# Performance work log

Measured on AMD Instinct MI355X. Metric: run time of the kernel, lower is better.

## Reference

```python
import jax, jax.numpy as jnp
import numpy as np

N, E, DIM, H = 50000, 800000, 128, 8
HD = DIM // H  # head_dim = 16
HID = 4 * DIM  # ffn hidden (hidden_dim_multiplier=4)


def setup_inputs() -> dict:
    key = jax.random.key(0)
    ks = jax.random.split(key, 12)
    s = 0.05
    return {
        "x": jax.random.normal(ks[0], (N, DIM), jnp.float32),
        "src": jax.random.randint(ks[1], (E,), 0, N, jnp.int32),
        "dst": jax.random.randint(ks[2], (E,), 0, N, jnp.int32),
        "fc_w": jax.random.normal(ks[3], (DIM, DIM), jnp.float32) * s,
        "fc_b": jax.random.normal(ks[4], (DIM,), jnp.float32) * s,
        "au_w": jax.random.normal(ks[5], (H, DIM), jnp.float32) * s,
        "au_b": jax.random.normal(ks[6], (H,), jnp.float32) * s,
        "av_w": jax.random.normal(ks[7], (H, DIM), jnp.float32) * s,
        "w1": jax.random.normal(ks[8], (HID, 4 * DIM), jnp.float32) * s,
        "b1": jax.random.normal(ks[9], (HID,), jnp.float32) * s,
        "w2": jax.random.normal(ks[10], (DIM, HID), jnp.float32) * s,
        "b2": jax.random.normal(ks[11], (DIM,), jnp.float32) * s,
    }


def reference(x, src, dst, fc_w, fc_b, au_w, au_b, av_w, w1, b1, w2, b2):
    h = x @ fc_w.T + fc_b                                   # [N, DIM]
    su = h @ au_w.T + au_b                                  # [N, H]
    sv = h @ av_w.T                                         # [N, H] (no bias)
    # u_add_v + LeakyReLU(0.2)
    scores = jax.nn.leaky_relu(su[src] + sv[dst], 0.2)      # [E, H]
    # edge_softmax grouped by destination node (stable)
    m = jax.ops.segment_max(scores, dst, num_segments=N)    # [N, H]
    ex = jnp.exp(scores - m[dst])
    den = jax.ops.segment_sum(ex, dst, num_segments=N)      # [N, H]
    probs = ex / den[dst]                                   # [E, H]
    # u_mul_e_sum over heads: x reshaped [N, head_dim, H]
    xh = h.reshape(N, HD, H)
    msg = jax.ops.segment_sum(xh[src] * probs[:, None, :], dst, num_segments=N)
    msg = msg.reshape(N, DIM)
    # copy_u_mean: mean of src features over incoming edges
    ones = jnp.ones((E,), h.dtype)
    in_deg = jax.ops.segment_sum(ones, dst, num_segments=N)   # [N]
    sum2 = jax.ops.segment_sum(xh[src], dst, num_segments=N)  # [N, HD, H]
    msg2 = (sum2 / jnp.maximum(in_deg, 1.0)[:, None, None]).reshape(N, DIM)
    # symmetric-norm message: norm = 1/sqrt(out_deg[src]*out_deg[dst])
    out_deg = jax.ops.segment_sum(ones, src, num_segments=N)  # [N]
    norm = 1.0 / jnp.sqrt(out_deg[src] * out_deg[dst])        # [E]
    msg3 = jax.ops.segment_sum(h[src] * norm[:, None], dst, num_segments=N)
    # combine + feed-forward (dropout=0 -> identity)
    cat = jnp.concatenate([h, msg, msg2, msg3], axis=1)       # [N, 4*DIM]
    f = jax.nn.gelu(cat @ w1.T + b1, approximate=False)
    return f @ w2.T + b2                                      # [N, DIM]
```

## Files before the change

kernel.cpp:

```cpp
#include <hip/hip_runtime.h>
#include <hip/hip_bf16.h>

#define NNODES 50000
#define NEDGES 800000
#define DIM 128
#define NH 8
#define HID 512
#define NB 196

typedef unsigned short ushort_t;
typedef unsigned int uint_t;
typedef __attribute__((ext_vector_type(8))) short bf16x8;
typedef __attribute__((ext_vector_type(4))) float f32x4;

__global__ __launch_bounds__(256) void convert_weights_kernel(
    const float* __restrict__ fc_w, const float* __restrict__ w1,
    const float* __restrict__ w2,
    ushort_t* __restrict__ fc_wb, ushort_t* __restrict__ w1b,
    ushort_t* __restrict__ w2b)
{
    int i = blockIdx.x * 256 + threadIdx.x;
    if (i < 16384)
        ((__hip_bfloat16*)fc_wb)[i] = __float2bfloat16(fc_w[i]);
    else if (i < 278528)
        ((__hip_bfloat16*)w1b)[i - 16384] = __float2bfloat16(w1[i - 16384]);
    else if (i < 344064)
        ((__hip_bfloat16*)w2b)[i - 278528] = __float2bfloat16(w2[i - 278528]);
}

template<int AF32, int OUTF32, int ACT>
__global__ __launch_bounds__(256, 4) void gemm_mfma(
    const void* A, int lda,
    const ushort_t* __restrict__ B, int ldb,
    const float* __restrict__ bias,
    void* C, int ldc, int row0,
    int M, int K)
{
    constexpr int BM = 128, BN = 128, BK = 32;
    __shared__ ushort_t As[BM * BK];
    __shared__ ushort_t Bs[BN * BK];

    const int t    = threadIdx.x;
    const int bm   = blockIdx.y * BM;
    const int bn   = blockIdx.x * BN;
    const int wid  = t >> 6, lane = t & 63;
    const int wrow = wid >> 1, wcol = wid & 1;
    const int qd   = lane >> 4, l16 = lane & 15;

    f32x4 acc[4][4];
#pragma unroll
    for (int i = 0; i < 4; ++i)
#pragma unroll
        for (int j = 0; j < 4; ++j) acc[i][j] = (f32x4){0.f, 0.f, 0.f, 0.f};

    for (int k0 = 0; k0 < K; k0 += BK) {
#pragma unroll
        for (int it = 0; it < 2; ++it) {
            const int v = it * 256 + t;
            const int r = v >> 2, q = v & 3;
            const int c = q ^ ((r >> 1) & 3);
            {
                const ushort_t* gB = B + (size_t)(bn + r) * ldb + k0 + c * 8;
                ushort_t* lB = &Bs[(it * 256 + wid * 64) * 8];
                __builtin_amdgcn_global_load_lds(
                    (const __attribute__((address_space(1))) uint_t*)gB,
                    (__attribute__((address_space(3))) uint_t*)lB, 16, 0, 0);
            }
            if (AF32) {
                int gr = bm + r;
                float4 f0 = make_float4(0.f, 0.f, 0.f, 0.f), f1 = f0;
                if (gr < M) {
                    const float* ap = (const float*)A + (size_t)gr * lda + k0 + c * 8;
                    f0 = *(const float4*)ap;
                    f1 = *(const float4*)(ap + 4);
                }
                __hip_bfloat16 tmp[8];
                tmp[0] = __float2bfloat16(f0.x); tmp[1] = __float2bfloat16(f0.y);
                tmp[2] = __float2bfloat16(f0.z); tmp[3] = __float2bfloat16(f0.w);
                tmp[4] = __float2bfloat16(f1.x); tmp[5] = __float2bfloat16(f1.y);
                tmp[6] = __float2bfloat16(f1.z); tmp[7] = __float2bfloat16(f1.w);
                *(uint4*)&As[(r * 4 + q) * 8] = *(const uint4*)tmp;
            } else {
                int gr = bm + r;
                if (gr >= M) gr = M - 1;
                const ushort_t* gA = (const ushort_t*)A + (size_t)gr * lda + k0 + c * 8;
                ushort_t* lA = &As[(it * 256 + wid * 64) * 8];
                __builtin_amdgcn_global_load_lds(
                    (const __attribute__((address_space(1))) uint_t*)gA,
                    (__attribute__((address_space(3))) uint_t*)lA, 16, 0, 0);
            }
        }
        __syncthreads();

        bf16x8 af[4], bfr[4];
#pragma unroll
        for (int mi = 0; mi < 4; ++mi) {
            const int row = wrow * 64 + mi * 16 + l16;
            af[mi] = *(const bf16x8*)&As[row * BK + ((qd ^ ((row >> 1) & 3)) * 8)];
        }
#pragma unroll
        for (int ni = 0; ni < 4; ++ni) {
            const int row = wcol * 64 + ni * 16 + l16;
            bfr[ni] = *(const bf16x8*)&Bs[row * BK + ((qd ^ ((row >> 1) & 3)) * 8)];
        }
#pragma unroll
        for (int mi = 0; mi < 4; ++mi)
#pragma unroll
            for (int ni = 0; ni < 4; ++ni)
                acc[mi][ni] = __builtin_amdgcn_mfma_f32_16x16x32_bf16(
                    af[mi], bfr[ni], acc[mi][ni], 0, 0, 0);
        __syncthreads();
    }

#pragma unroll
    for (int mi = 0; mi < 4; ++mi) {
#pragma unroll
        for (int r = 0; r < 4; ++r) {
            int lrow = wrow * 64 + mi * 16 + qd * 4 + r;
            int grow = bm + lrow;
            if (grow >= M) continue;
#pragma unroll
            for (int ni = 0; ni < 4; ++ni) {
                int gc = bn + wcol * 64 + ni * 16 + l16;
                float v = acc[mi][ni][r] + bias[gc];
                if (ACT == 1) v = 0.5f * v * (1.f + erff(v * 0.70710678118654752f));
                size_t off = (size_t)(row0 + grow) * ldc + gc;
                if (OUTF32) ((float*)C)[off] = v;
                else ((__hip_bfloat16*)C)[off] = __float2bfloat16(v);
            }
        }
    }
}

__global__ __launch_bounds__(256) void attn_scores_kernel(
    const ushort_t* __restrict__ hb,
    const float* __restrict__ au_w, const float* __restrict__ au_b,
    const float* __restrict__ av_w,
    float* __restrict__ su, float* __restrict__ sv, int N)
{
    const int wave = threadIdx.x >> 6;
    const int lane = threadIdx.x & 63;
    const int n = blockIdx.x * 4 + wave;
    if (n >= N) return;

    const float h0 = __bfloat162float(((const __hip_bfloat16*)hb)[(size_t)n * DIM + lane]);
    const float h1 = __bfloat162float(((const __hip_bfloat16*)hb)[(size_t)n * DIM + 64 + lane]);

    float au[NH], av[NH];
#pragma unroll
    for (int hh = 0; hh < NH; ++hh) {
        au[hh] = h0 * au_w[hh * DIM + lane] + h1 * au_w[hh * DIM + 64 + lane];
        av[hh] = h0 * av_w[hh * DIM + lane] + h1 * av_w[hh * DIM + 64 + lane];
    }
#pragma unroll
    for (int off = 32; off >= 1; off >>= 1) {
#pragma unroll
        for (int hh = 0; hh < NH; ++hh) {
            au[hh] += __shfl_down(au[hh], off, 64);
            av[hh] += __shfl_down(av[hh], off, 64);
        }
    }
    if (lane == 0) {
#pragma unroll
        for (int hh = 0; hh < NH; ++hh) {
            su[(size_t)n * NH + hh] = au[hh] + au_b[hh];
            sv[(size_t)n * NH + hh] = av[hh];
        }
    }
}

__global__ __launch_bounds__(256) void degree_count_kernel(
    const int* __restrict__ src, const int* __restrict__ dst,
    float* __restrict__ out_deg, int* __restrict__ in_cnt, int E)
{
    int e = blockIdx.x * 256 + threadIdx.x;
    if (e >= E) return;
    unsafeAtomicAdd(&out_deg[src[e]], 1.f);
    atomicAdd(&in_cnt[dst[e]], 1);
}

__global__ __launch_bounds__(256) void block_sum_kernel(
    const int* __restrict__ cnt, int* __restrict__ bsum)
{
    const int lane = threadIdx.x & 63, wid = threadIdx.x >> 6;
    int i = blockIdx.x * 256 + threadIdx.x;
    int v = (i < NNODES) ? cnt[i] : 0;
#pragma unroll
    for (int off = 32; off >= 1; off >>= 1) v += __shfl_down(v, off, 64);
    __shared__ int ws_[4];
    if (lane == 0) ws_[wid] = v;
    __syncthreads();
    if (threadIdx.x == 0) bsum[blockIdx.x] = ws_[0] + ws_[1] + ws_[2] + ws_[3];
}

__global__ __launch_bounds__(256) void block_scan_kernel(
    const int* __restrict__ bsum, int* __restrict__ boff)
{
    __shared__ int sb[256];
    const int t = threadIdx.x;
    int v = (t < NB) ? bsum[t] : 0;
    sb[t] = v;
    __syncthreads();
    for (int off = 1; off < 256; off <<= 1) {
        int u = (t >= off) ? sb[t - off] : 0;
        __syncthreads();
        sb[t] += u;
        __syncthreads();
    }
    if (t < NB) boff[t] = (t == 0) ? 0 : sb[t - 1];
}

__global__ __launch_bounds__(256) void final_scan_kernel(
    const int* __restrict__ cnt, const int* __restrict__ boff,
    int* __restrict__ rowstart)
{
    __shared__ int sb[256];
    const int t = threadIdx.x;
    const int b = blockIdx.x;
    int i = b * 256 + t;
    int v = (i < NNODES) ? cnt[i] : 0;
    sb[t] = v;
    __syncthreads();
    for (int off = 1; off < 256; off <<= 1) {
        int u = (t >= off) ? sb[t - off] : 0;
        __syncthreads();
        sb[t] += u;
        __syncthreads();
    }
    if (i < NNODES) rowstart[i] = boff[b] + sb[t] - v;
    if (b == 0 && t == 0) rowstart[NNODES] = NEDGES;
}

__global__ __launch_bounds__(256) void fill_csr_kernel(
    const int* __restrict__ src, const int* __restrict__ dst,
    const int* __restrict__ rowstart, int* __restrict__ cursor,
    int* __restrict__ esrc, int E)
{
    int e = blockIdx.x * 256 + threadIdx.x;
    if (e >= E) return;
    int d = dst[e];
    int pos = rowstart[d] + atomicAdd(&cursor[d], 1);
    esrc[pos] = src[e];
}

__device__ __forceinline__ float bf_lo(uint_t v) {
    union { uint_t i; float f; } c; c.i = v << 16; return c.f;
}
__device__ __forceinline__ float bf_hi(uint_t v) {
    union { uint_t i; float f; } c; c.i = v & 0xffff0000u; return c.f;
}
__device__ __forceinline__ void st_bf2(ushort_t* p, float a, float b) {
    __hip_bfloat16 ba = __float2bfloat16(a), bb = __float2bfloat16(b);
    uint_t v = (uint_t)(*(ushort_t*)&ba) | ((uint_t)(*(ushort_t*)&bb) << 16);
    *(uint_t*)p = v;
}

__global__ __launch_bounds__(256) void gather_aggregate_kernel(
    const int* __restrict__ rowstart, const int* __restrict__ esrc,
    const ushort_t* __restrict__ hb,
    const float* __restrict__ su, const float* __restrict__ sv,
    const float* __restrict__ out_deg,
    ushort_t* __restrict__ cat, int N)
{
    const int wave = threadIdx.x >> 6;
    const int lane = threadIdx.x & 63;
    const int n = blockIdx.x * 4 + wave;
    if (n >= N) return;

    const int d0 = lane << 1;
    const int h0 = d0 & 7;

    const int e0  = rowstart[n];
    const int deg = rowstart[n + 1] - e0;
    const float2 svv = *(const float2*)(sv + (size_t)n * NH + h0);
    const float od_d = out_deg[n];

    int es = 0;
    if (deg > 0) es = esrc[e0 + (lane < deg ? lane : deg - 1)];

    float den0 = 0.f, den1 = 0.f;
    float m0 = 0.f, m1 = 0.f, s0 = 0.f, s1 = 0.f, n0 = 0.f, n1 = 0.f;

    const int degm = deg & ~3;
    for (int j = 0; j < degm; j += 4) {
        int s4[4]; float2 su4[4]; float od4[4]; uint_t hv4[4];
#pragma unroll
        for (int u = 0; u < 4; ++u) {
            int jj = j + u;
            s4[u] = (jj < 64) ? __shfl(es, jj, 64) : esrc[e0 + jj];
        }
#pragma unroll
        for (int u = 0; u < 4; ++u) {
            su4[u] = *(const float2*)(su + (size_t)s4[u] * NH + h0);
            od4[u] = out_deg[s4[u]];
            hv4[u] = *(const uint_t*)(hb + (size_t)s4[u] * DIM + d0);
        }
#pragma unroll
        for (int u = 0; u < 4; ++u) {
            float sc0 = su4[u].x + svv.x; sc0 = sc0 < 0.f ? 0.2f * sc0 : sc0;
            float sc1 = su4[u].y + svv.y; sc1 = sc1 < 0.f ? 0.2f * sc1 : sc1;
            float ex0 = __expf(sc0), ex1 = __expf(sc1);
            den0 += ex0; den1 += ex1;
            float nrm = rsqrtf(od4[u] * od_d);
            float hs0 = bf_lo(hv4[u]), hs1 = bf_hi(hv4[u]);
            m0 += hs0 * ex0; m1 += hs1 * ex1;
            s0 += hs0;       s1 += hs1;
            n0 += hs0 * nrm; n1 += hs1 * nrm;
        }
    }
    for (int j = degm; j < deg; ++j) {
        int s = (j < 64) ? __shfl(es, j, 64) : esrc[e0 + j];
        float2 suv = *(const float2*)(su + (size_t)s * NH + h0);
        float odv  = out_deg[s];
        uint_t hv  = *(const uint_t*)(hb + (size_t)s * DIM + d0);
        float sc0 = suv.x + svv.x; sc0 = sc0 < 0.f ? 0.2f * sc0 : sc0;
        float sc1 = suv.y + svv.y; sc1 = sc1 < 0.f ? 0.2f * sc1 : sc1;
        float ex0 = __expf(sc0), ex1 = __expf(sc1);
        den0 += ex0; den1 += ex1;
        float nrm = rsqrtf(odv * od_d);
        float hs0 = bf_lo(hv), hs1 = bf_hi(hv);
        m0 += hs0 * ex0; m1 += hs1 * ex1;
        s0 += hs0;       s1 += hs1;
        n0 += hs0 * nrm; n1 += hs1 * nrm;
    }

    const float inv = 1.f / fmaxf((float)deg, 1.f);
    const float r0 = den0 > 0.f ? 1.f / den0 : 0.f;
    const float r1 = den1 > 0.f ? 1.f / den1 : 0.f;
    ushort_t* row = cat + (size_t)n * 512;
    *(uint_t*)(row + d0) = *(const uint_t*)(hb + (size_t)n * DIM + d0);
    st_bf2(row + 128 + d0, m0 * r0, m1 * r1);
    st_bf2(row + 256 + d0, s0 * inv, s1 * inv);
    st_bf2(row + 384 + d0, n0, n1);
}

extern "C" void kernel_launch(void* const* d_in, const int* in_sizes, int n_in,
                              void* d_out, int out_size, void* d_ws, size_t ws_size,
                              hipStream_t stream)
{
    const float* x    = (const float*)d_in[0];
    const int*   src  = (const int*)d_in[1];
    const int*   dst  = (const int*)d_in[2];
    const float* fc_w = (const float*)d_in[3];
    const float* fc_b = (const float*)d_in[4];
    const float* au_w = (const float*)d_in[5];
    const float* au_b = (const float*)d_in[6];
    const float* av_w = (const float*)d_in[7];
    const float* w1   = (const float*)d_in[8];
    const float* b1   = (const float*)d_in[9];
    const float* w2   = (const float*)d_in[10];
    const float* b2   = (const float*)d_in[11];
    float* out = (float*)d_out;

    const int N = NNODES, E = NEDGES;

    char* w = (char*)d_ws;
    ushort_t* fc_wb = (ushort_t*)w;  w += (size_t)DIM * DIM * 2;
    ushort_t* w1b   = (ushort_t*)w;  w += (size_t)HID * 512 * 2;
    ushort_t* w2b   = (ushort_t*)w;  w += (size_t)DIM * HID * 2;
    ushort_t* hb    = (ushort_t*)w;  w += (size_t)N * DIM * 2;
    ushort_t* cat   = (ushort_t*)w;  w += (size_t)N * 512 * 2;
    float* su       = (float*)w;     w += (size_t)N * NH * 4;
    float* sv       = (float*)w;     w += (size_t)N * NH * 4;
    float* out_deg  = (float*)w;     w += (size_t)N * 4;
    int*   in_cnt   = (int*)w;       w += (size_t)N * 4;
    int*   cursor   = (int*)w;       w += (size_t)N * 4;
    int*   rowstart = (int*)w;       w += (size_t)(N + 16) * 4;
    int*   bsum     = (int*)w;       w += (size_t)256 * 4;
    int*   boff     = (int*)w;       w += (size_t)256 * 4;
    int*   esrc     = (int*)w;       w += (size_t)E * 4;
    size_t base_bytes = (size_t)(w - (char*)d_ws);
    ushort_t* fbuf  = (ushort_t*)w;

    const int CHR = (ws_size >= base_bytes + (size_t)N * 512 * 2 + 1024) ? N : 12500;

    (void)hipMemsetAsync(out_deg, 0, (size_t)N * 3 * 4, stream);

    convert_weights_kernel<<<1344, 256, 0, stream>>>(fc_w, w1, w2, fc_wb, w1b, w2b);

    {
        dim3 g(1, (N + 127) / 128);
        gemm_mfma<1, 0, 0><<<g, 256, 0, stream>>>(x, DIM, fc_wb, DIM, fc_b,
                                                  hb, DIM, 0, N, DIM);
    }
    attn_scores_kernel<<<(N + 3) / 4, 256, 0, stream>>>(hb, au_w, au_b, av_w, su, sv, N);
    degree_count_kernel<<<(E + 255) / 256, 256, 0, stream>>>(src, dst, out_deg, in_cnt, E);
    block_sum_kernel<<<NB, 256, 0, stream>>>(in_cnt, bsum);
    block_scan_kernel<<<1, 256, 0, stream>>>(bsum, boff);
    final_scan_kernel<<<NB, 256, 0, stream>>>(in_cnt, boff, rowstart);
    fill_csr_kernel<<<(E + 255) / 256, 256, 0, stream>>>(src, dst, rowstart, cursor, esrc, E);
    gather_aggregate_kernel<<<(N + 3) / 4, 256, 0, stream>>>(
        rowstart, esrc, hb, su, sv, out_deg, cat, N);

    for (int c0 = 0; c0 < N; c0 += CHR) {
        int Mc = (c0 + CHR <= N) ? CHR : N - c0;
        {
            dim3 g(HID / 128, (Mc + 127) / 128);
            gemm_mfma<0, 0, 1><<<g, 256, 0, stream>>>(cat + (size_t)c0 * 512, 512,
                                                      w1b, 512, b1,
                                                      fbuf, HID, 0, Mc, 512);
        }
        {
            dim3 g(DIM / 128, (Mc + 127) / 128);
            gemm_mfma<0, 1, 0><<<g, 256, 0, stream>>>(fbuf, HID, w2b, HID, b2,
                                                      out, DIM, c0, Mc, 512);
        }
    }
}
```

Baseline: 425.5 us.

## Triple-buffer bf16 GEMM LDS loads with async prefetch and drop XOR swizzle

The bf16-input GEMM path now keeps three LDS buffers and prefetches tiles two k-steps ahead with global_load_lds. It waits with explicit vmcnt counts and uses one barrier per iteration instead of two, so global loads overlap MFMA work. The XOR swizzle on LDS layout is removed from both paths, which simplifies addressing but may add LDS bank conflicts. Occupancy hint drops from 4 to 3 blocks because shared memory grows threefold.

```diff
diff --git a/kernel.cpp b/kernel.cpp
--- a/kernel.cpp
+++ b/kernel.cpp
@@ -12,6 +12,9 @@
 typedef unsigned int uint_t;
 typedef __attribute__((ext_vector_type(8))) short bf16x8;
 typedef __attribute__((ext_vector_type(4))) float f32x4;
+
+#define WAITVM4 asm volatile("s_waitcnt vmcnt(4)" ::: "memory")
+#define WAITVM0 asm volatile("s_waitcnt vmcnt(0)" ::: "memory")
 
 __global__ __launch_bounds__(256) void convert_weights_kernel(
     const float* __restrict__ fc_w, const float* __restrict__ w1,
@@ -29,7 +32,7 @@
 }
 
 template<int AF32, int OUTF32, int ACT>
-__global__ __launch_bounds__(256, 4) void gemm_mfma(
+__global__ __launch_bounds__(256, 3) void gemm_mfma(
     const void* A, int lda,
     const ushort_t* __restrict__ B, int ldb,
     const float* __restrict__ bias,
@@ -37,8 +40,8 @@
     int M, int K)
 {
     constexpr int BM = 128, BN = 128, BK = 32;
-    __shared__ ushort_t As[BM * BK];
-    __shared__ ushort_t Bs[BN * BK];
+    __shared__ ushort_t As[3][BM * BK];
+    __shared__ ushort_t Bs[3][BN * BK];
 
     const int t    = threadIdx.x;
     const int bm   = blockIdx.y * BM;
@@ -47,30 +50,31 @@
     const int wrow = wid >> 1, wcol = wid & 1;
     const int qd   = lane >> 4, l16 = lane & 15;
 
+    const ushort_t* Abf = (const ushort_t*)A;
+
     f32x4 acc[4][4];
 #pragma unroll
     for (int i = 0; i < 4; ++i)
 #pragma unroll
         for (int j = 0; j < 4; ++j) acc[i][j] = (f32x4){0.f, 0.f, 0.f, 0.f};
 
-    for (int k0 = 0; k0 < K; k0 += BK) {
-#pragma unroll
-        for (int it = 0; it < 2; ++it) {
-            const int v = it * 256 + t;
-            const int r = v >> 2, q = v & 3;
-            const int c = q ^ ((r >> 1) & 3);
-            {
-                const ushort_t* gB = B + (size_t)(bn + r) * ldb + k0 + c * 8;
-                ushort_t* lB = &Bs[(it * 256 + wid * 64) * 8];
-                __builtin_amdgcn_global_load_lds(
-                    (const __attribute__((address_space(1))) uint_t*)gB,
-                    (__attribute__((address_space(3))) uint_t*)lB, 16, 0, 0);
-            }
-            if (AF32) {
+    if (AF32) {
+        for (int k0 = 0; k0 < K; k0 += BK) {
+#pragma unroll
+            for (int it = 0; it < 2; ++it) {
+                const int v = it * 256 + t;
+                const int r = v >> 2, q = v & 3;
+                {
+                    const ushort_t* gB = B + (size_t)(bn + r) * ldb + k0 + q * 8;
+                    ushort_t* lB = &Bs[0][(it * 256 + wid * 64) * 8];
+                    __builtin_amdgcn_global_load_lds(
+                        (const __attribute__((address_space(1))) uint_t*)gB,
+                        (__attribute__((address_space(3))) uint_t*)lB, 16, 0, 0);
+                }
                 int gr = bm + r;
                 float4 f0 = make_float4(0.f, 0.f, 0.f, 0.f), f1 = f0;
                 if (gr < M) {
-                    const float* ap = (const float*)A + (size_t)gr * lda + k0 + c * 8;
+                    const float* ap = (const float*)A + (size_t)gr * lda + k0 + q * 8;
                     f0 = *(const float4*)ap;
                     f1 = *(const float4*)(ap + 4);
                 }
@@ -79,37 +83,78 @@
                 tmp[2] = __float2bfloat16(f0.z); tmp[3] = __float2bfloat16(f0.w);
                 tmp[4] = __float2bfloat16(f1.x); tmp[5] = __float2bfloat16(f1.y);
                 tmp[6] = __float2bfloat16(f1.z); tmp[7] = __float2bfloat16(f1.w);
-                *(uint4*)&As[(r * 4 + q) * 8] = *(const uint4*)tmp;
-            } else {
+                *(uint4*)&As[0][(r * 4 + q) * 8] = *(const uint4*)tmp;
+            }
+            __syncthreads();
+
+            bf16x8 af[4], bfr[4];
+#pragma unroll
+            for (int mi = 0; mi < 4; ++mi) {
+                const int row = wrow * 64 + mi * 16 + l16;
+                af[mi] = *(const bf16x8*)&As[0][row * BK + qd * 8];
+            }
+#pragma unroll
+            for (int ni = 0; ni < 4; ++ni) {
+                const int row = wcol * 64 + ni * 16 + l16;
+                bfr[ni] = *(const bf16x8*)&Bs[0][row * BK + qd * 8];
+            }
+#pragma unroll
+            for (int mi = 0; mi < 4; ++mi)
+#pragma unroll
+                for (int ni = 0; ni < 4; ++ni)
+                    acc[mi][ni] = __builtin_amdgcn_mfma_f32_16x16x32_bf16(
+                        af[mi], bfr[ni], acc[mi][ni], 0, 0, 0);
+            __syncthreads();
+        }
+    } else {
+        auto stage = [&](int k0, int bufi) {
+#pragma unroll
+            for (int it = 0; it < 2; ++it) {
+                const int v = it * 256 + t;
+                const int r = v >> 2, q = v & 3;
                 int gr = bm + r;
                 if (gr >= M) gr = M - 1;
-                const ushort_t* gA = (const ushort_t*)A + (size_t)gr * lda + k0 + c * 8;
-                ushort_t* lA = &As[(it * 256 + wid * 64) * 8];
+                const ushort_t* gA = Abf + (size_t)gr * lda + k0 + q * 8;
+                ushort_t* lA = &As[bufi][(it * 256 + wid * 64) * 8];
                 __builtin_amdgcn_global_load_lds(
                     (const __attribute__((address_space(1))) uint_t*)gA,
                     (__attribute__((address_space(3))) uint_t*)lA, 16, 0, 0);
-            }
-        }
-        __syncthreads();
-
-        bf16x8 af[4], bfr[4];
-#pragma unroll
-        for (int mi = 0; mi < 4; ++mi) {
-            const int row = wrow * 64 + mi * 16 + l16;
-            af[mi] = *(const bf16x8*)&As[row * BK + ((qd ^ ((row >> 1) & 3)) * 8)];
-        }
-#pragma unroll
-        for (int ni = 0; ni < 4; ++ni) {
-            const int row = wcol * 64 + ni * 16 + l16;
-            bfr[ni] = *(const bf16x8*)&Bs[row * BK + ((qd ^ ((row >> 1) & 3)) * 8)];
-        }
-#pragma unroll
-        for (int mi = 0; mi < 4; ++mi)
-#pragma unroll
-            for (int ni = 0; ni < 4; ++ni)
-                acc[mi][ni] = __builtin_amdgcn_mfma_f32_16x16x32_bf16(
-                    af[mi], bfr[ni], acc[mi][ni], 0, 0, 0);
-        __syncthreads();
+                const ushort_t* gB = B + (size_t)(bn + r) * ldb + k0 + q * 8;
+                ushort_t* lB = &Bs[bufi][(it * 256 + wid * 64) * 8];
+                __builtin_amdgcn_global_load_lds(
+                    (const __attribute__((address_space(1))) uint_t*)gB,
+                    (__attribute__((address_space(3))) uint_t*)lB, 16, 0, 0);
+            }
+        };
+
+        const int nk = K >> 5;
+        stage(0, 0);
+        stage(BK, 1);
+
+        for (int kb = 0; kb < nk; ++kb) {
+            if (kb + 1 < nk) { WAITVM4; } else { WAITVM0; }
+            __builtin_amdgcn_s_barrier();
+            if (kb + 2 < nk) stage((kb + 2) * BK, (kb + 2) % 3);
+
+            const int b = kb % 3;
+            bf16x8 af[4], bfr[4];
+#pragma unroll
+            for (int mi = 0; mi < 4; ++mi) {
+                const int row = wrow * 64 + mi * 16 + l16;
+                af[mi] = *(const bf16x8*)&As[b][row * BK + qd * 8];
+            }
+#pragma unroll
+            for (int ni = 0; ni < 4; ++ni) {
+                const int row = wcol * 64 + ni * 16 + l16;
+                bfr[ni] = *(const bf16x8*)&Bs[b][row * BK + qd * 8];
+            }
+#pragma unroll
+            for (int mi = 0; mi < 4; ++mi)
+#pragma unroll
+                for (int ni = 0; ni < 4; ++ni)
+                    acc[mi][ni] = __builtin_amdgcn_mfma_f32_16x16x32_bf16(
+                        af[mi], bfr[ni], acc[mi][ni], 0, 0, 0);
+        }
     }
 
 #pragma unroll
```

Measured after the change: 443.3 us. 4.2% more time.
